# Kernel tuning notes

Hardware: AMD Instinct MI355X
Metric: run time of the kernel (lower is better)

The kernel has to match this reference:

```python
import jax, jax.numpy as jnp
import numpy as np

N_OUT, D_OUT, N_IN, D_IN, N_ROUTING = 32, 32, 2048, 16, 3
BATCH = 64


def squash(x, axis=-1):
    norm2 = jnp.sum(x * x, axis=axis, keepdims=True)
    scale = norm2 / (1.0 + norm2) / jnp.sqrt(norm2)
    return scale * x


def setup_inputs() -> dict:
    key = jax.random.key(0)
    k_u, k_w = jax.random.split(key)
    u = jax.random.normal(k_u, (BATCH, N_IN, D_IN), dtype=jnp.float32)
    stdv = 1.0 / np.sqrt(N_IN)
    W = jax.random.uniform(k_w, (N_IN, D_IN, N_OUT * D_OUT), dtype=jnp.float32,
                           minval=-stdv, maxval=stdv)
    return {"u": u, "W": W}


def reference(u, W):
    B = u.shape[0]
    # uhat[b,n,o,k] = sum_i u[b,n,i] * W[n,i,o*k]
    uhat = jnp.einsum('bni,nij->bnj', u, W).reshape(B, N_IN, N_OUT, D_OUT)
    b = jnp.zeros((B, N_IN, N_OUT), dtype=u.dtype)
    v = None
    for r in range(N_ROUTING):
        c = jax.nn.softmax(b, axis=-1)            # [B, nIn, nOut]
        s = jnp.einsum('bno,bnok->bok', c, uhat)  # [B, nOut, dOut]
        v = squash(s)
        if r != N_ROUTING - 1:
            a = jnp.einsum('bnok,bok->bno', uhat, v)  # agreement
            b = b + a
    return v
```

## Files before the change

### kernel.cpp

```cpp
#include <hip/hip_runtime.h>
#include <math.h>

#define N_OUT 32
#define D_OUT 32
#define N_IN 2048
#define D_IN 16
#define BATCH 64
#define J 1024

typedef __attribute__((ext_vector_type(8))) short short8;
typedef __attribute__((ext_vector_type(4))) float f32x4;
typedef __attribute__((ext_vector_type(16))) float f32x16;

__device__ __forceinline__ unsigned short f2bf(float f) {
  unsigned int x = __float_as_uint(f);
  return (unsigned short)((x + 0x7FFFu + ((x >> 16) & 1u)) >> 16);
}

__device__ __forceinline__ int wp(int u) { return u ^ ((u >> 3) & 1); }

__device__ __forceinline__ void pack_col(const float* wc, uint4& d0, uint4& d1) {
  d0.x = (unsigned)f2bf(wc[0])  | ((unsigned)f2bf(wc[1])  << 16);
  d0.y = (unsigned)f2bf(wc[2])  | ((unsigned)f2bf(wc[3])  << 16);
  d0.z = (unsigned)f2bf(wc[4])  | ((unsigned)f2bf(wc[5])  << 16);
  d0.w = (unsigned)f2bf(wc[6])  | ((unsigned)f2bf(wc[7])  << 16);
  d1.x = (unsigned)f2bf(wc[8])  | ((unsigned)f2bf(wc[9])  << 16);
  d1.y = (unsigned)f2bf(wc[10]) | ((unsigned)f2bf(wc[11]) << 16);
  d1.z = (unsigned)f2bf(wc[12]) | ((unsigned)f2bf(wc[13]) << 16);
  d1.w = (unsigned)f2bf(wc[14]) | ((unsigned)f2bf(wc[15]) << 16);
}

__device__ __forceinline__ short8 pack_u(const float4& a4, const float4& b4) {
  short8 B;
  B[0] = (short)f2bf(a4.x); B[1] = (short)f2bf(a4.y);
  B[2] = (short)f2bf(a4.z); B[3] = (short)f2bf(a4.w);
  B[4] = (short)f2bf(b4.x); B[5] = (short)f2bf(b4.y);
  B[6] = (short)f2bf(b4.z); B[7] = (short)f2bf(b4.w);
  return B;
}

__device__ __forceinline__ f32x16 zero16() {
  f32x16 z;
  #pragma unroll
  for (int i = 0; i < 16; ++i) z[i] = 0.f;
  return z;
}


template<int MODE>
__global__ __launch_bounds__(1024, 1)
void pass0w_kernel(const float* __restrict__ uf, const float* __restrict__ Wf,
                   short* __restrict__ Wbf, short* __restrict__ ubf,
                   float* __restrict__ part)
{
  __shared__ uint4 Wt[4][2048];

  const int t  = threadIdx.x;
  const int l  = t & 63;
  const int w  = t >> 6;
  const int bid = blockIdx.x;
  const int bh = (bid >> 3) & 1;
  const int cx = (bid & 7) | ((bid >> 4) << 3);
  const int n0 = cx * 16;

  const int bl = l & 31;
  const int b  = bh * 32 + bl;
  const int kh = l >> 5;
  const bool wq = (MODE == 0) && ((t >> 9) == bh);
  const bool uq = (MODE == 0) && (w == 0);

  int aoff[2];
  #pragma unroll
  for (int q = 0; q < 2; ++q) aoff[q] = wp(2 * (w * 64 + q * 32 + bl) + kh);

  f32x16 acc[2];
  acc[0] = zero16();
  acc[1] = zero16();

  short8 Ba, Bb;

  {
    float wa[16], wb[16];
    const float* sa = Wf + (size_t)n0 * (D_IN * J) + t;
    const float* sb = Wf + (size_t)(n0 + 1) * (D_IN * J) + t;
    #pragma unroll
    for (int i = 0; i < 16; ++i) wa[i] = sa[i * J];
    #pragma unroll
    for (int i = 0; i < 16; ++i) wb[i] = sb[i * J];
    const float* upa = uf + ((size_t)b * N_IN + n0) * D_IN + kh * 8;
    float4 ua0 = *reinterpret_cast<const float4*>(upa);
    float4 ua1 = *reinterpret_cast<const float4*>(upa + 4);
    const float* upb = uf + ((size_t)b * N_IN + n0 + 1) * D_IN + kh * 8;
    float4 ub0 = *reinterpret_cast<const float4*>(upb);
    float4 ub1 = *reinterpret_cast<const float4*>(upb + 4);
    __builtin_amdgcn_sched_barrier(0);
    uint4 d0, d1;
    pack_col(wa, d0, d1);
    Wt[0][wp(2 * t)] = d0;
    Wt[0][wp(2 * t + 1)] = d1;
    if (wq) {
      uint4* g = reinterpret_cast<uint4*>(Wbf + (size_t)n0 * (D_IN * J));
      g[wp(2 * t)] = d0;
      g[wp(2 * t + 1)] = d1;
    }
    pack_col(wb, d0, d1);
    Wt[1][wp(2 * t)] = d0;
    Wt[1][wp(2 * t + 1)] = d1;
    if (wq) {
      uint4* g = reinterpret_cast<uint4*>(Wbf + (size_t)(n0 + 1) * (D_IN * J));
      g[wp(2 * t)] = d0;
      g[wp(2 * t + 1)] = d1;
    }
    Ba = pack_u(ua0, ua1);
    Bb = pack_u(ub0, ub1);
    if (uq) {
      *reinterpret_cast<short8*>(ubf + ((size_t)b * N_IN + n0) * D_IN + kh * 8) = Ba;
      *reinterpret_cast<short8*>(ubf + ((size_t)b * N_IN + n0 + 1) * D_IN + kh * 8) = Bb;
    }
  }
  __syncthreads();

  for (int ss = 0; ss < 8; ++ss) {
    const int na = n0 + 2 * ss;
    const int p = ss & 1;
    const bool more = (ss + 1 < 8);

    float wa[16], wb[16];
    float4 ua0 = {0,0,0,0}, ua1 = {0,0,0,0}, ub0 = {0,0,0,0}, ub1 = {0,0,0,0};
    if (more) {
      const float* sa = Wf + (size_t)(na + 2) * (D_IN * J) + t;
      const float* sb = Wf + (size_t)(na + 3) * (D_IN * J) + t;
      #pragma unroll
      for (int i = 0; i < 16; ++i) wa[i] = sa[i * J];
      #pragma unroll
      for (int i = 0; i < 16; ++i) wb[i] = sb[i * J];
      const float* upa = uf + ((size_t)b * N_IN + na + 2) * D_IN + kh * 8;
      ua0 = *reinterpret_cast<const float4*>(upa);
      ua1 = *reinterpret_cast<const float4*>(upa + 4);
      const float* upb = uf + ((size_t)b * N_IN + na + 3) * D_IN + kh * 8;
      ub0 = *reinterpret_cast<const float4*>(upb);
      ub1 = *reinterpret_cast<const float4*>(upb + 4);
      __builtin_amdgcn_sched_barrier(0);
    }

    {
      const uint4* bufA = Wt[2 * p];
      const uint4* bufB = Wt[2 * p + 1];
      #pragma unroll
      for (int q = 0; q < 2; ++q) {
        short8 A = *reinterpret_cast<const short8*>(&bufA[aoff[q]]);
        acc[q] = __builtin_amdgcn_mfma_f32_32x32x16_bf16(A, Ba, acc[q], 0, 0, 0);
      }
      #pragma unroll
      for (int q = 0; q < 2; ++q) {
        short8 A = *reinterpret_cast<const short8*>(&bufB[aoff[q]]);
        acc[q] = __builtin_amdgcn_mfma_f32_32x32x16_bf16(A, Bb, acc[q], 0, 0, 0);
      }
    }

    short8 Bna, Bnb;
    if (more) {
      uint4 d0, d1;
      pack_col(wa, d0, d1);
      Wt[2 * (1 - p)][wp(2 * t)] = d0;
      Wt[2 * (1 - p)][wp(2 * t + 1)] = d1;
      if (wq) {
        uint4* g = reinterpret_cast<uint4*>(Wbf + (size_t)(na + 2) * (D_IN * J));
        g[wp(2 * t)] = d0;
        g[wp(2 * t + 1)] = d1;
      }
      pack_col(wb, d0, d1);
      Wt[2 * (1 - p) + 1][wp(2 * t)] = d0;
      Wt[2 * (1 - p) + 1][wp(2 * t + 1)] = d1;
      if (wq) {
        uint4* g = reinterpret_cast<uint4*>(Wbf + (size_t)(na + 3) * (D_IN * J));
        g[wp(2 * t)] = d0;
        g[wp(2 * t + 1)] = d1;
      }
      Bna = pack_u(ua0, ua1);
      Bnb = pack_u(ub0, ub1);
      if (uq) {
        *reinterpret_cast<short8*>(ubf + ((size_t)b * N_IN + na + 2) * D_IN + kh * 8) = Bna;
        *reinterpret_cast<short8*>(ubf + ((size_t)b * N_IN + na + 3) * D_IN + kh * 8) = Bnb;
      }
      Ba = Bna;
      Bb = Bnb;
    }
    __syncthreads();
  }

  #pragma unroll
  for (int q = 0; q < 2; ++q) {
    #pragma unroll
    for (int r = 0; r < 16; ++r) {
      int j = w * 64 + q * 32 + (r & 3) + 8 * (r >> 2) + 4 * kh;
      part[((size_t)cx * J + j) * 64 + b] = acc[q][r];
    }
  }
}

__global__ __launch_bounds__(1024, 1)
void pass1w_kernel(const short* __restrict__ Wbf, const short* __restrict__ ubf,
                   const float* __restrict__ vin, float* __restrict__ part)
{
  __shared__ uint4 Wt[2][2048];
  __shared__ float al[2][32][33];

  const int t  = threadIdx.x;
  const int l  = t & 63;
  const int w  = t >> 6;
  const int bid = blockIdx.x;
  const int bh = (bid >> 3) & 1;
  const int cx = (bid & 7) | ((bid >> 4) << 3);
  const int n0 = cx * 16;

  const int bl = l & 31;
  const int b  = bh * 32 + bl;
  const int kh = l >> 5;

  int aoff[2];
  #pragma unroll
  for (int q = 0; q < 2; ++q) aoff[q] = wp(2 * (w * 64 + q * 32 + bl) + kh);

  unsigned vb[16];
  #pragma unroll
  for (int q = 0; q < 2; ++q) {
    #pragma unroll
    for (int g = 0; g < 4; ++g) {
      int j = w * 64 + q * 32 + 8 * g + 4 * kh;
      f32x4 v4 = *reinterpret_cast<const f32x4*>(vin + (size_t)b * J + j);
      vb[q * 8 + 2 * g]     = (unsigned)f2bf(v4[0]) | ((unsigned)f2bf(v4[1]) << 16);
      vb[q * 8 + 2 * g + 1] = (unsigned)f2bf(v4[2]) | ((unsigned)f2bf(v4[3]) << 16);
    }
  }

  f32x16 acc[2];
  acc[0] = zero16();
  acc[1] = zero16();

  short8 B;
  {
    const uint4* src = reinterpret_cast<const uint4*>(Wbf + (size_t)n0 * (D_IN * J));
    Wt[0][t] = src[t];
    Wt[0][t + 1024] = src[t + 1024];
    B = *reinterpret_cast<const short8*>(ubf + ((size_t)b * N_IN + n0) * D_IN + kh * 8);
  }
  __syncthreads();

  for (int nn = 0; nn < 16; ++nn) {
    const int n = n0 + nn;
    const int cur = nn & 1, nxt = cur ^ 1, par = nn & 1;
    const bool more = (nn + 1 < 16);

    uint4 s0, s1;
    short8 Bn;
    if (more) {
      const uint4* src = reinterpret_cast<const uint4*>(Wbf + (size_t)(n + 1) * (D_IN * J));
      s0 = src[t];
      s1 = src[t + 1024];
      Bn = *reinterpret_cast<const short8*>(ubf + ((size_t)b * N_IN + n + 1) * D_IN + kh * 8);
      __builtin_amdgcn_sched_barrier(0);
    }

    f32x16 C[2];
    {
      const uint4* buf = Wt[cur];
      #pragma unroll
      for (int q = 0; q < 2; ++q) {
        short8 A = *reinterpret_cast<const short8*>(&buf[aoff[q]]);
        C[q] = __builtin_amdgcn_mfma_f32_32x32x16_bf16(A, B, zero16(), 0, 0, 0);
      }
    }

    #pragma unroll
    for (int q = 0; q < 2; ++q) {
      float s = 0.f;
      #pragma unroll
      for (int r = 0; r < 16; ++r) {
        unsigned u = vb[q * 8 + (r >> 1)];
        float v = (r & 1) ? __uint_as_float(u & 0xffff0000u)
                          : __uint_as_float(u << 16);
        s += C[q][r] * v;
      }
      s += __shfl_xor(s, 32);
      if (l < 32) al[par][w * 2 + q][bl] = s;
    }

    if (more) {
      Wt[nxt][t] = s0;
      Wt[nxt][t + 1024] = s1;
    }

    __syncthreads();
    {
      int sb = t >> 5, so = t & 31;
      float x = al[par][so][sb];
      float m = x;
      #pragma unroll
      for (int k = 1; k < 32; k <<= 1) m = fmaxf(m, __shfl_xor(m, k));
      float e = __expf(x - m);
      float sm = e;
      #pragma unroll
      for (int k = 1; k < 32; k <<= 1) sm += __shfl_xor(sm, k);
      al[par][so][sb] = e / sm;
    }
    __syncthreads();
    #pragma unroll
    for (int q = 0; q < 2; ++q) {
      float c = al[par][w * 2 + q][bl];
      #pragma unroll
      for (int r = 0; r < 16; ++r) acc[q][r] += C[q][r] * c;
    }
    B = Bn;
  }

  #pragma unroll
  for (int q = 0; q < 2; ++q) {
    #pragma unroll
    for (int r = 0; r < 16; ++r) {
      int j = w * 64 + q * 32 + (r & 3) + 8 * (r >> 2) + 4 * kh;
      part[((size_t)cx * J + j) * 64 + b] = acc[q][r];
    }
  }
}

template<bool HAS_V, int MODE, int NCHUNK>
__global__ __launch_bounds__(1024, 1)
void pass_kernel(const float* __restrict__ uf, const float* __restrict__ Wf,
                 short* __restrict__ Wbf, short* __restrict__ ubf,
                 const float* __restrict__ vin, float* __restrict__ part)
{
  __shared__ uint4 Wt[2][2048];
  __shared__ float al[2][32][18];

  const int t  = threadIdx.x;
  const int l  = t & 63;
  const int w  = t >> 6;
  const int bid = blockIdx.x;
  const int bq = (bid >> 3) & 3;
  const int cx = (bid & 7) | ((bid >> 5) << 3);
  const int n0 = cx * NCHUNK;

  const int bl = l & 15;
  const int b  = bq * 16 + bl;
  const int h  = l >> 4;
  const int hA = h & 1;
  const bool ld = (l < 32);

  f32x4 vf[4];
  if (HAS_V) {
    #pragma unroll
    for (int q = 0; q < 4; ++q)
      vf[q] = *reinterpret_cast<const f32x4*>(vin + (size_t)b * J + (w*4+q)*16 + h*4);
  }

  int aoff[4];
  #pragma unroll
  for (int q = 0; q < 4; ++q) aoff[q] = wp(2 * ((w*4+q) * 16 + bl) + hA);

  f32x4 acc[4];
  #pragma unroll
  for (int q = 0; q < 4; ++q) acc[q] = f32x4{0.f, 0.f, 0.f, 0.f};

  short8 Bcur = short8{0,0,0,0,0,0,0,0};
  {
    float wc[16];
    const float* wsrc = Wf + (size_t)n0 * (D_IN * J) + t;
    #pragma unroll
    for (int i = 0; i < 16; ++i) wc[i] = wsrc[i * J];
    float4 a4 = {0,0,0,0}, b4 = {0,0,0,0};
    if (ld) {
      const float* up = uf + ((size_t)b * N_IN + n0) * D_IN + hA * 8;
      a4 = *reinterpret_cast<const float4*>(up);
      b4 = *reinterpret_cast<const float4*>(up + 4);
    }
    __builtin_amdgcn_sched_barrier(0);
    uint4 d0, d1;
    pack_col(wc, d0, d1);
    Wt[0][wp(2 * t)] = d0;
    Wt[0][wp(2 * t + 1)] = d1;
    if (ld) Bcur = pack_u(a4, b4);
  }
  __syncthreads();

  for (int nn = 0; nn < NCHUNK; ++nn) {
    const int n = n0 + nn;
    const int cur = nn & 1, nxt = cur ^ 1, par = nn & 1;
    const bool more = (nn + 1 < NCHUNK);

    float wc[16];
    float4 a4 = {0,0,0,0}, b4 = {0,0,0,0};
    if (more) {
      const float* wsrc = Wf + (size_t)(n + 1) * (D_IN * J) + t;
      #pragma unroll
      for (int i = 0; i < 16; ++i) wc[i] = wsrc[i * J];
      if (ld) {
        const float* up = uf + ((size_t)b * N_IN + n + 1) * D_IN + hA * 8;
        a4 = *reinterpret_cast<const float4*>(up);
        b4 = *reinterpret_cast<const float4*>(up + 4);
      }
      __builtin_amdgcn_sched_barrier(0);
    }

    f32x4 C[4];
    const uint4* buf = Wt[cur];
    #pragma unroll
    for (int q = 0; q < 4; ++q) {
      short8 A = short8{0,0,0,0,0,0,0,0};
      if (ld) A = *reinterpret_cast<const short8*>(&buf[aoff[q]]);
      f32x4 z = f32x4{0.f, 0.f, 0.f, 0.f};
      C[q] = __builtin_amdgcn_mfma_f32_16x16x32_bf16(A, Bcur, z, 0, 0, 0);
    }

    short8 Bn = short8{0,0,0,0,0,0,0,0};
    if (more && ld) Bn = pack_u(a4, b4);

    if (HAS_V) {
      float ap[2] = {0.f, 0.f};
      #pragma unroll
      for (int q = 0; q < 4; ++q) {
        float s = C[q][0]*vf[q][0] + C[q][1]*vf[q][1] + C[q][2]*vf[q][2] + C[q][3]*vf[q][3];
        ap[q >> 1] += s;
      }
      #pragma unroll
      for (int p = 0; p < 2; ++p) {
        float s = ap[p];
        s += __shfl_xor(s, 16);
        s += __shfl_xor(s, 32);
        if (l < 16) al[par][w * 2 + p][l] = s;
      }
      if (more) {
        uint4 d0, d1;
        pack_col(wc, d0, d1);
        Wt[nxt][wp(2 * t)] = d0;
        Wt[nxt][wp(2 * t + 1)] = d1;
      }
      __syncthreads();
      if (t < 512) {
        int sb = t >> 5, so = t & 31;
        float x = al[par][so][sb];
        float m = x;
        #pragma unroll
        for (int k = 1; k < 32; k <<= 1) m = fmaxf(m, __shfl_xor(m, k));
        float e = __expf(x - m);
        float sm = e;
        #pragma unroll
        for (int k = 1; k < 32; k <<= 1) sm += __shfl_xor(sm, k);
        al[par][so][sb] = e / sm;
      }
      __syncthreads();
      #pragma unroll
      for (int q = 0; q < 4; ++q) {
        float c = al[par][(w * 4 + q) >> 1][bl];
        acc[q] += C[q] * c;
      }
    } else {
      #pragma unroll
      for (int q = 0; q < 4; ++q) acc[q] += C[q];
      if (more) {
        uint4 d0, d1;
        pack_col(wc, d0, d1);
        Wt[nxt][wp(2 * t)] = d0;
        Wt[nxt][wp(2 * t + 1)] = d1;
      }
      __syncthreads();
    }
    Bcur = Bn;
  }

  #pragma unroll
  for (int q = 0; q < 4; ++q) {
    int jbase = (w * 4 + q) * 16 + h * 4;
    #pragma unroll
    for (int r = 0; r < 4; ++r)
      part[((size_t)cx * J + jbase + r) * 64 + b] = acc[q][r];
  }
}

template<int NC>
__global__ __launch_bounds__(1024)
void rsq_kernel(const float* __restrict__ part, const float* __restrict__ addv,
                float* __restrict__ out, float prescale)
{
  __shared__ float ps[2][32][17];
  __shared__ float vl[32][17];
  __shared__ float scl[16];
  const int o  = blockIdx.x >> 2;
  const int bq = blockIdx.x & 3;
  const int t  = threadIdx.x;
  {
    const int bb = t & 15;
    const int kk = (t >> 4) & 31;
    const int ch = t >> 9;
    const float* p = part + (size_t)(o * 32 + kk) * 64 + bq * 16 + bb;
    float s = 0.f;
    #pragma unroll 8
    for (int c = ch * (NC / 2); c < (ch + 1) * (NC / 2); ++c)
      s += p[(size_t)c * (J * 64)];
    ps[ch][kk][bb] = s;
  }
  __syncthreads();
  if (t < 512) {
    int kk = t >> 4, bb = t & 15;
    vl[kk][bb] = (ps[0][kk][bb] + ps[1][kk][bb]) * prescale;
  }
  __syncthreads();
  if (t < 16) {
    float n2 = 0.f;
    #pragma unroll
    for (int k = 0; k < 32; ++k) { float x = vl[k][t]; n2 += x * x; }
    scl[t] = sqrtf(n2) / (1.f + n2);
  }
  __syncthreads();
  if (t < 512) {
    int bb = t >> 5, kk = t & 31;
    int idx = (bq * 16 + bb) * J + o * 32 + kk;
    float val = scl[bb] * vl[kk][bb];
    if (addv) val += addv[idx];
    out[idx] = val;
  }
}

extern "C" void kernel_launch(void* const* d_in, const int* in_sizes, int n_in,
                              void* d_out, int out_size, void* d_ws, size_t ws_size,
                              hipStream_t stream)
{
  const float* u = (const float*)d_in[0];
  const float* W = (const float*)d_in[1];
  float* out = (float*)d_out;
  char* ws = (char*)d_ws;

  const size_t WBF_B = (size_t)N_IN * D_IN * J * 2;
  const size_t UBF_B = (size_t)BATCH * N_IN * D_IN * 2;
  const size_t SMALL = 2ull * BATCH * J * 4;
  const size_t PART128 = (size_t)128 * J * 64 * 4;
  const size_t PART64  = (size_t)64 * J * 64 * 4;

  if (ws_size >= WBF_B + UBF_B + PART128 + SMALL) {
    short* Wbf = (short*)ws;
    short* ubf = (short*)(ws + WBF_B);
    float* part = (float*)(ws + WBF_B + UBF_B);
    float* v0 = part + (size_t)128 * J * 64;
    float* vs = v0 + BATCH * J;
    pass0w_kernel<0><<<256, 1024, 0, stream>>>(u, W, Wbf, ubf, part);
    rsq_kernel<128><<<128, 1024, 0, stream>>>(part, nullptr, v0, 1.f / 32.f);
    pass1w_kernel<<<256, 1024, 0, stream>>>(Wbf, ubf, v0, part);
    rsq_kernel<128><<<128, 1024, 0, stream>>>(part, v0, vs, 1.f);
    pass1w_kernel<<<256, 1024, 0, stream>>>(Wbf, ubf, vs, part);
    rsq_kernel<128><<<128, 1024, 0, stream>>>(part, nullptr, out, 1.f);
  } else if (ws_size >= PART64 + SMALL) {
    float* part = (float*)ws;
    float* v0 = part + (size_t)64 * J * 64;
    float* vs = v0 + BATCH * J;
    pass_kernel<false, 2, 32><<<256, 1024, 0, stream>>>(u, W, nullptr, nullptr, nullptr, part);
    rsq_kernel<64><<<128, 1024, 0, stream>>>(part, nullptr, v0, 1.f / 32.f);
    pass_kernel<true, 2, 32><<<256, 1024, 0, stream>>>(u, W, nullptr, nullptr, v0, part);
    rsq_kernel<64><<<128, 1024, 0, stream>>>(part, v0, vs, 1.f);
    pass_kernel<true, 2, 32><<<256, 1024, 0, stream>>>(u, W, nullptr, nullptr, vs, part);
    rsq_kernel<64><<<128, 1024, 0, stream>>>(part, nullptr, out, 1.f);
  } else {
    float* part = (float*)ws;
    float* v0 = part + (size_t)16 * J * 64;
    float* vs = v0 + BATCH * J;
    pass_kernel<false, 2, 128><<<64, 1024, 0, stream>>>(u, W, nullptr, nullptr, nullptr, part);
    rsq_kernel<16><<<128, 1024, 0, stream>>>(part, nullptr, v0, 1.f / 32.f);
    pass_kernel<true, 2, 128><<<64, 1024, 0, stream>>>(u, W, nullptr, nullptr, v0, part);
    rsq_kernel<16><<<128, 1024, 0, stream>>>(part, v0, vs, 1.f);
    pass_kernel<true, 2, 128><<<64, 1024, 0, stream>>>(u, W, nullptr, nullptr, vs, part);
    rsq_kernel<16><<<128, 1024, 0, stream>>>(part, nullptr, out, 1.f);
  }
}
```

Measured before the change: 159.3 us.

## Replace LDS-staged pass0 with small-block wave-shuffle kernel over 1024 blocks

```diff
diff --git a/kernel.cpp b/kernel.cpp
--- a/kernel.cpp
+++ b/kernel.cpp
@@ -46,154 +46,92 @@
   return z;
 }
 
-
-template<int MODE>
-__global__ __launch_bounds__(1024, 1)
-void pass0w_kernel(const float* __restrict__ uf, const float* __restrict__ Wf,
+template<int NCHUNK>
+__global__ __launch_bounds__(256, 4)
+void pass0s_kernel(const float* __restrict__ uf, const float* __restrict__ Wf,
                    short* __restrict__ Wbf, short* __restrict__ ubf,
                    float* __restrict__ part)
 {
-  __shared__ uint4 Wt[4][2048];
-
-  const int t  = threadIdx.x;
-  const int l  = t & 63;
-  const int w  = t >> 6;
+  const int t   = threadIdx.x;
+  const int l   = t & 63;
+  const int wv  = t >> 6;
   const int bid = blockIdx.x;
-  const int bh = (bid >> 3) & 1;
-  const int cx = (bid & 7) | ((bid >> 4) << 3);
-  const int n0 = cx * 16;
-
-  const int bl = l & 31;
-  const int b  = bh * 32 + bl;
-  const int kh = l >> 5;
-  const bool wq = (MODE == 0) && ((t >> 9) == bh);
-  const bool uq = (MODE == 0) && (w == 0);
-
-  int aoff[2];
-  #pragma unroll
-  for (int q = 0; q < 2; ++q) aoff[q] = wp(2 * (w * 64 + q * 32 + bl) + kh);
+  const int bjg = bid & 3;
+  const int bh  = (bid >> 2) & 1;
+  const int cx  = bid >> 3;
+  const int jg  = bjg * 4 + wv;
+  const int j0  = jg * 64;
+  const int bl  = l & 31;
+  const int b   = bh * 32 + bl;
+  const int kh  = l >> 5;
+  const int n0  = cx * NCHUNK;
+  const bool emitW = (bh == 0);
+  const bool emitU = (jg == 0);
 
   f32x16 acc[2];
   acc[0] = zero16();
   acc[1] = zero16();
 
-  short8 Ba, Bb;
-
-  {
-    float wa[16], wb[16];
-    const float* sa = Wf + (size_t)n0 * (D_IN * J) + t;
-    const float* sb = Wf + (size_t)(n0 + 1) * (D_IN * J) + t;
-    #pragma unroll
-    for (int i = 0; i < 16; ++i) wa[i] = sa[i * J];
-    #pragma unroll
-    for (int i = 0; i < 16; ++i) wb[i] = sb[i * J];
-    const float* upa = uf + ((size_t)b * N_IN + n0) * D_IN + kh * 8;
-    float4 ua0 = *reinterpret_cast<const float4*>(upa);
-    float4 ua1 = *reinterpret_cast<const float4*>(upa + 4);
-    const float* upb = uf + ((size_t)b * N_IN + n0 + 1) * D_IN + kh * 8;
-    float4 ub0 = *reinterpret_cast<const float4*>(upb);
-    float4 ub1 = *reinterpret_cast<const float4*>(upb + 4);
-    __builtin_amdgcn_sched_barrier(0);
+  float wcA[16], wcB[16];
+  float4 uA0, uA1, uB0, uB1;
+
+  auto load_n = [&](float (&wc)[16], float4& u0, float4& u1, int n) {
+    const float* ws = Wf + (size_t)n * (D_IN * J) + j0 + l;
+    #pragma unroll
+    for (int i = 0; i < 16; ++i) wc[i] = ws[i * J];
+    const float* up = uf + ((size_t)b * N_IN + n) * D_IN + kh * 8;
+    u0 = *reinterpret_cast<const float4*>(up);
+    u1 = *reinterpret_cast<const float4*>(up + 4);
+  };
+
+  auto body = [&](const float (&wc)[16], const float4& u0, const float4& u1, int n) {
     uint4 d0, d1;
-    pack_col(wa, d0, d1);
-    Wt[0][wp(2 * t)] = d0;
-    Wt[0][wp(2 * t + 1)] = d1;
-    if (wq) {
-      uint4* g = reinterpret_cast<uint4*>(Wbf + (size_t)n0 * (D_IN * J));
-      g[wp(2 * t)] = d0;
-      g[wp(2 * t + 1)] = d1;
-    }
-    pack_col(wb, d0, d1);
-    Wt[1][wp(2 * t)] = d0;
-    Wt[1][wp(2 * t + 1)] = d1;
-    if (wq) {
-      uint4* g = reinterpret_cast<uint4*>(Wbf + (size_t)(n0 + 1) * (D_IN * J));
-      g[wp(2 * t)] = d0;
-      g[wp(2 * t + 1)] = d1;
-    }
-    Ba = pack_u(ua0, ua1);
-    Bb = pack_u(ub0, ub1);
-    if (uq) {
-      *reinterpret_cast<short8*>(ubf + ((size_t)b * N_IN + n0) * D_IN + kh * 8) = Ba;
-      *reinterpret_cast<short8*>(ubf + ((size_t)b * N_IN + n0 + 1) * D_IN + kh * 8) = Bb;
-    }
-  }
-  __syncthreads();
-
-  for (int ss = 0; ss < 8; ++ss) {
-    const int na = n0 + 2 * ss;
-    const int p = ss & 1;
-    const bool more = (ss + 1 < 8);
-
-    float wa[16], wb[16];
-    float4 ua0 = {0,0,0,0}, ua1 = {0,0,0,0}, ub0 = {0,0,0,0}, ub1 = {0,0,0,0};
-    if (more) {
-      const float* sa = Wf + (size_t)(na + 2) * (D_IN * J) + t;
-      const float* sb = Wf + (size_t)(na + 3) * (D_IN * J) + t;
-      #pragma unroll
-      for (int i = 0; i < 16; ++i) wa[i] = sa[i * J];
-      #pragma unroll
-      for (int i = 0; i < 16; ++i) wb[i] = sb[i * J];
-      const float* upa = uf + ((size_t)b * N_IN + na + 2) * D_IN + kh * 8;
-      ua0 = *reinterpret_cast<const float4*>(upa);
-      ua1 = *reinterpret_cast<const float4*>(upa + 4);
-      const float* upb = uf + ((size_t)b * N_IN + na + 3) * D_IN + kh * 8;
-      ub0 = *reinterpret_cast<const float4*>(upb);
-      ub1 = *reinterpret_cast<const float4*>(upb + 4);
+    pack_col(wc, d0, d1);
+    if (emitW) {
+      uint4* g = reinterpret_cast<uint4*>(Wbf + (size_t)n * (D_IN * J));
+      g[wp(2 * (j0 + l))] = d0;
+      g[wp(2 * (j0 + l) + 1)] = d1;
+    }
+    short8 B = pack_u(u0, u1);
+    if (emitU)
+      *reinterpret_cast<short8*>(ubf + ((size_t)b * N_IN + n) * D_IN + kh * 8) = B;
+    const unsigned* p0 = reinterpret_cast<const unsigned*>(&d0);
+    const unsigned* p1 = reinterpret_cast<const unsigned*>(&d1);
+    #pragma unroll
+    for (int q = 0; q < 2; ++q) {
+      int src = q * 32 + bl;
+      unsigned a[4];
+      #pragma unroll
+      for (int e = 0; e < 4; ++e) {
+        unsigned lo = (unsigned)__shfl((int)p0[e], src);
+        unsigned hi = (unsigned)__shfl((int)p1[e], src);
+        a[e] = kh ? hi : lo;
+      }
+      short8 A = *reinterpret_cast<const short8*>(a);
+      acc[q] = __builtin_amdgcn_mfma_f32_32x32x16_bf16(A, B, acc[q], 0, 0, 0);
+    }
+  };
+
+  load_n(wcA, uA0, uA1, n0);
+
+  #pragma unroll
+  for (int ss = 0; ss < NCHUNK; ++ss) {
+    const int n = n0 + ss;
+    const bool cur_is_A = ((ss & 1) == 0);
+    if (ss + 1 < NCHUNK) {
+      if (cur_is_A) load_n(wcB, uB0, uB1, n + 1);
+      else          load_n(wcA, uA0, uA1, n + 1);
       __builtin_amdgcn_sched_barrier(0);
     }
-
-    {
-      const uint4* bufA = Wt[2 * p];
-      const uint4* bufB = Wt[2 * p + 1];
-      #pragma unroll
-      for (int q = 0; q < 2; ++q) {
-        short8 A = *reinterpret_cast<const short8*>(&bufA[aoff[q]]);
-        acc[q] = __builtin_amdgcn_mfma_f32_32x32x16_bf16(A, Ba, acc[q], 0, 0, 0);
-      }
-      #pragma unroll
-      for (int q = 0; q < 2; ++q) {
-        short8 A = *reinterpret_cast<const short8*>(&bufB[aoff[q]]);
-        acc[q] = __builtin_amdgcn_mfma_f32_32x32x16_bf16(A, Bb, acc[q], 0, 0, 0);
-      }
-    }
-
-    short8 Bna, Bnb;
-    if (more) {
-      uint4 d0, d1;
-      pack_col(wa, d0, d1);
-      Wt[2 * (1 - p)][wp(2 * t)] = d0;
-      Wt[2 * (1 - p)][wp(2 * t + 1)] = d1;
-      if (wq) {
-        uint4* g = reinterpret_cast<uint4*>(Wbf + (size_t)(na + 2) * (D_IN * J));
-        g[wp(2 * t)] = d0;
-        g[wp(2 * t + 1)] = d1;
-      }
-      pack_col(wb, d0, d1);
-      Wt[2 * (1 - p) + 1][wp(2 * t)] = d0;
-      Wt[2 * (1 - p) + 1][wp(2 * t + 1)] = d1;
-      if (wq) {
-        uint4* g = reinterpret_cast<uint4*>(Wbf + (size_t)(na + 3) * (D_IN * J));
-        g[wp(2 * t)] = d0;
-        g[wp(2 * t + 1)] = d1;
-      }
-      Bna = pack_u(ua0, ua1);
-      Bnb = pack_u(ub0, ub1);
-      if (uq) {
-        *reinterpret_cast<short8*>(ubf + ((size_t)b * N_IN + na + 2) * D_IN + kh * 8) = Bna;
-        *reinterpret_cast<short8*>(ubf + ((size_t)b * N_IN + na + 3) * D_IN + kh * 8) = Bnb;
-      }
-      Ba = Bna;
-      Bb = Bnb;
-    }
-    __syncthreads();
+    if (cur_is_A) body(wcA, uA0, uA1, n);
+    else          body(wcB, uB0, uB1, n);
   }
 
   #pragma unroll
   for (int q = 0; q < 2; ++q) {
     #pragma unroll
     for (int r = 0; r < 16; ++r) {
-      int j = w * 64 + q * 32 + (r & 3) + 8 * (r >> 2) + 4 * kh;
+      int j = j0 + q * 32 + (r & 3) + 8 * (r >> 2) + 4 * kh;
       part[((size_t)cx * J + j) * 64 + b] = acc[q][r];
     }
   }
@@ -542,7 +480,7 @@
     float* part = (float*)(ws + WBF_B + UBF_B);
     float* v0 = part + (size_t)128 * J * 64;
     float* vs = v0 + BATCH * J;
-    pass0w_kernel<0><<<256, 1024, 0, stream>>>(u, W, Wbf, ubf, part);
+    pass0s_kernel<16><<<1024, 256, 0, stream>>>(u, W, Wbf, ubf, part);
     rsq_kernel<128><<<128, 1024, 0, stream>>>(part, nullptr, v0, 1.f / 32.f);
     pass1w_kernel<<<256, 1024, 0, stream>>>(Wbf, ubf, v0, part);
     rsq_kernel<128><<<128, 1024, 0, stream>>>(part, v0, vs, 1.f);
```

New measurement: 197.5 us. 1.24x slower.

## Fuse routing passes into one cooperative persistent kernel with grid syncs

Applied to the files above, without the earlier changes.

```diff
diff --git a/kernel.cpp b/kernel.cpp
--- a/kernel.cpp
+++ b/kernel.cpp
@@ -1,5 +1,8 @@
 #include <hip/hip_runtime.h>
+#include <hip/hip_cooperative_groups.h>
 #include <math.h>
+
+namespace cg = cooperative_groups;
 
 #define N_OUT 32
 #define D_OUT 32
@@ -47,14 +50,12 @@
 }
 
 
-template<int MODE>
-__global__ __launch_bounds__(1024, 1)
-void pass0w_kernel(const float* __restrict__ uf, const float* __restrict__ Wf,
-                   short* __restrict__ Wbf, short* __restrict__ ubf,
-                   float* __restrict__ part)
-{
-  __shared__ uint4 Wt[4][2048];
-
+
+__device__ __forceinline__
+void pass0_phase(const float* __restrict__ uf, const float* __restrict__ Wf,
+                 short* __restrict__ Wbf, short* __restrict__ ubf,
+                 float* __restrict__ part, uint4 (&Wt)[4][2048])
+{
   const int t  = threadIdx.x;
   const int l  = t & 63;
   const int w  = t >> 6;
@@ -66,8 +67,8 @@
   const int bl = l & 31;
   const int b  = bh * 32 + bl;
   const int kh = l >> 5;
-  const bool wq = (MODE == 0) && ((t >> 9) == bh);
-  const bool uq = (MODE == 0) && (w == 0);
+  const bool wq = ((t >> 9) == bh);
+  const bool uq = (w == 0);
 
   int aoff[2];
   #pragma unroll
@@ -199,13 +200,11 @@
   }
 }
 
-__global__ __launch_bounds__(1024, 1)
-void pass1w_kernel(const short* __restrict__ Wbf, const short* __restrict__ ubf,
-                   const float* __restrict__ vin, float* __restrict__ part)
-{
-  __shared__ uint4 Wt[2][2048];
-  __shared__ float al[2][32][33];
-
+__device__ __forceinline__
+void pass1_phase(const short* __restrict__ Wbf, const short* __restrict__ ubf,
+                 const float* __restrict__ vin, float* __restrict__ part,
+                 uint4 (&Wt)[4][2048], float (&al)[2][32][33])
+{
   const int t  = threadIdx.x;
   const int l  = t & 63;
   const int w  = t >> 6;
@@ -324,169 +323,15 @@
   }
 }
 
-template<bool HAS_V, int MODE, int NCHUNK>
-__global__ __launch_bounds__(1024, 1)
-void pass_kernel(const float* __restrict__ uf, const float* __restrict__ Wf,
-                 short* __restrict__ Wbf, short* __restrict__ ubf,
-                 const float* __restrict__ vin, float* __restrict__ part)
-{
-  __shared__ uint4 Wt[2][2048];
-  __shared__ float al[2][32][18];
-
-  const int t  = threadIdx.x;
-  const int l  = t & 63;
-  const int w  = t >> 6;
+__device__ __forceinline__
+void rsq_phase(const float* __restrict__ part, const float* __restrict__ addv,
+               float* __restrict__ out, float prescale,
+               float (&ps)[2][32][17], float (&vl)[32][17], float (&scl)[16])
+{
   const int bid = blockIdx.x;
-  const int bq = (bid >> 3) & 3;
-  const int cx = (bid & 7) | ((bid >> 5) << 3);
-  const int n0 = cx * NCHUNK;
-
-  const int bl = l & 15;
-  const int b  = bq * 16 + bl;
-  const int h  = l >> 4;
-  const int hA = h & 1;
-  const bool ld = (l < 32);
-
-  f32x4 vf[4];
-  if (HAS_V) {
-    #pragma unroll
-    for (int q = 0; q < 4; ++q)
-      vf[q] = *reinterpret_cast<const f32x4*>(vin + (size_t)b * J + (w*4+q)*16 + h*4);
-  }
-
-  int aoff[4];
-  #pragma unroll
-  for (int q = 0; q < 4; ++q) aoff[q] = wp(2 * ((w*4+q) * 16 + bl) + hA);
-
-  f32x4 acc[4];
-  #pragma unroll
-  for (int q = 0; q < 4; ++q) acc[q] = f32x4{0.f, 0.f, 0.f, 0.f};
-
-  short8 Bcur = short8{0,0,0,0,0,0,0,0};
-  {
-    float wc[16];
-    const float* wsrc = Wf + (size_t)n0 * (D_IN * J) + t;
-    #pragma unroll
-    for (int i = 0; i < 16; ++i) wc[i] = wsrc[i * J];
-    float4 a4 = {0,0,0,0}, b4 = {0,0,0,0};
-    if (ld) {
-      const float* up = uf + ((size_t)b * N_IN + n0) * D_IN + hA * 8;
-      a4 = *reinterpret_cast<const float4*>(up);
-      b4 = *reinterpret_cast<const float4*>(up + 4);
-    }
-    __builtin_amdgcn_sched_barrier(0);
-    uint4 d0, d1;
-    pack_col(wc, d0, d1);
-    Wt[0][wp(2 * t)] = d0;
-    Wt[0][wp(2 * t + 1)] = d1;
-    if (ld) Bcur = pack_u(a4, b4);
-  }
-  __syncthreads();
-
-  for (int nn = 0; nn < NCHUNK; ++nn) {
-    const int n = n0 + nn;
-    const int cur = nn & 1, nxt = cur ^ 1, par = nn & 1;
-    const bool more = (nn + 1 < NCHUNK);
-
-    float wc[16];
-    float4 a4 = {0,0,0,0}, b4 = {0,0,0,0};
-    if (more) {
-      const float* wsrc = Wf + (size_t)(n + 1) * (D_IN * J) + t;
-      #pragma unroll
-      for (int i = 0; i < 16; ++i) wc[i] = wsrc[i * J];
-      if (ld) {
-        const float* up = uf + ((size_t)b * N_IN + n + 1) * D_IN + hA * 8;
-        a4 = *reinterpret_cast<const float4*>(up);
-        b4 = *reinterpret_cast<const float4*>(up + 4);
-      }
-      __builtin_amdgcn_sched_barrier(0);
-    }
-
-    f32x4 C[4];
-    const uint4* buf = Wt[cur];
-    #pragma unroll
-    for (int q = 0; q < 4; ++q) {
-      short8 A = short8{0,0,0,0,0,0,0,0};
-      if (ld) A = *reinterpret_cast<const short8*>(&buf[aoff[q]]);
-      f32x4 z = f32x4{0.f, 0.f, 0.f, 0.f};
-      C[q] = __builtin_amdgcn_mfma_f32_16x16x32_bf16(A, Bcur, z, 0, 0, 0);
-    }
-
-    short8 Bn = short8{0,0,0,0,0,0,0,0};
-    if (more && ld) Bn = pack_u(a4, b4);
-
-    if (HAS_V) {
-      float ap[2] = {0.f, 0.f};
-      #pragma unroll
-      for (int q = 0; q < 4; ++q) {
-        float s = C[q][0]*vf[q][0] + C[q][1]*vf[q][1] + C[q][2]*vf[q][2] + C[q][3]*vf[q][3];
-        ap[q >> 1] += s;
-      }
-      #pragma unroll
-      for (int p = 0; p < 2; ++p) {
-        float s = ap[p];
-        s += __shfl_xor(s, 16);
-        s += __shfl_xor(s, 32);
-        if (l < 16) al[par][w * 2 + p][l] = s;
-      }
-      if (more) {
-        uint4 d0, d1;
-        pack_col(wc, d0, d1);
-        Wt[nxt][wp(2 * t)] = d0;
-        Wt[nxt][wp(2 * t + 1)] = d1;
-      }
-      __syncthreads();
-      if (t < 512) {
-        int sb = t >> 5, so = t & 31;
-        float x = al[par][so][sb];
-        float m = x;
-        #pragma unroll
-        for (int k = 1; k < 32; k <<= 1) m = fmaxf(m, __shfl_xor(m, k));
-        float e = __expf(x - m);
-        float sm = e;
-        #pragma unroll
-        for (int k = 1; k < 32; k <<= 1) sm += __shfl_xor(sm, k);
-        al[par][so][sb] = e / sm;
-      }
-      __syncthreads();
-      #pragma unroll
-      for (int q = 0; q < 4; ++q) {
-        float c = al[par][(w * 4 + q) >> 1][bl];
-        acc[q] += C[q] * c;
-      }
-    } else {
-      #pragma unroll
-      for (int q = 0; q < 4; ++q) acc[q] += C[q];
-      if (more) {
-        uint4 d0, d1;
-        pack_col(wc, d0, d1);
-        Wt[nxt][wp(2 * t)] = d0;
-        Wt[nxt][wp(2 * t + 1)] = d1;
-      }
-      __syncthreads();
-    }
-    Bcur = Bn;
-  }
-
-  #pragma unroll
-  for (int q = 0; q < 4; ++q) {
-    int jbase = (w * 4 + q) * 16 + h * 4;
-    #pragma unroll
-    for (int r = 0; r < 4; ++r)
-      part[((size_t)cx * J + jbase + r) * 64 + b] = acc[q][r];
-  }
-}
-
-template<int NC>
-__global__ __launch_bounds__(1024)
-void rsq_kernel(const float* __restrict__ part, const float* __restrict__ addv,
-                float* __restrict__ out, float prescale)
-{
-  __shared__ float ps[2][32][17];
-  __shared__ float vl[32][17];
-  __shared__ float scl[16];
-  const int o  = blockIdx.x >> 2;
-  const int bq = blockIdx.x & 3;
+  if (bid >= 128) return;
+  const int o  = bid >> 2;
+  const int bq = bid & 3;
   const int t  = threadIdx.x;
   {
     const int bb = t & 15;
@@ -495,7 +340,7 @@
     const float* p = part + (size_t)(o * 32 + kk) * 64 + bq * 16 + bb;
     float s = 0.f;
     #pragma unroll 8
-    for (int c = ch * (NC / 2); c < (ch + 1) * (NC / 2); ++c)
+    for (int c = ch * 64; c < (ch + 1) * 64; ++c)
       s += p[(size_t)c * (J * 64)];
     ps[ch][kk][bb] = s;
   }
@@ -519,6 +364,62 @@
     if (addv) val += addv[idx];
     out[idx] = val;
   }
+  __syncthreads();
+}
+
+__global__ __launch_bounds__(1024)
+void mega_kernel(const float* __restrict__ uf, const float* __restrict__ Wf,
+                 short* __restrict__ Wbf, short* __restrict__ ubf,
+                 float* __restrict__ part, float* __restrict__ v0,
+                 float* __restrict__ vs, float* __restrict__ out)
+{
+  __shared__ uint4 Wt[4][2048];
+  __shared__ float al[2][32][33];
+  __shared__ float ps[2][32][17];
+  __shared__ float vl[32][17];
+  __shared__ float scl[16];
+
+  cg::grid_group grid = cg::this_grid();
+
+  pass0_phase(uf, Wf, Wbf, ubf, part, Wt);
+  grid.sync();
+  rsq_phase(part, nullptr, v0, 1.f / 32.f, ps, vl, scl);
+  grid.sync();
+  pass1_phase(Wbf, ubf, v0, part, Wt, al);
+  grid.sync();
+  rsq_phase(part, v0, vs, 1.f, ps, vl, scl);
+  grid.sync();
+  pass1_phase(Wbf, ubf, vs, part, Wt, al);
+  grid.sync();
+  rsq_phase(part, nullptr, out, 1.f, ps, vl, scl);
+}
+
+__global__ __launch_bounds__(1024, 1)
+void pass0w_kernel(const float* __restrict__ uf, const float* __restrict__ Wf,
+                   short* __restrict__ Wbf, short* __restrict__ ubf,
+                   float* __restrict__ part)
+{
+  __shared__ uint4 Wt[4][2048];
+  pass0_phase(uf, Wf, Wbf, ubf, part, Wt);
+}
+
+__global__ __launch_bounds__(1024, 1)
+void pass1w_kernel(const short* __restrict__ Wbf, const short* __restrict__ ubf,
+                   const float* __restrict__ vin, float* __restrict__ part)
+{
+  __shared__ uint4 Wt[4][2048];
+  __shared__ float al[2][32][33];
+  pass1_phase(Wbf, ubf, vin, part, Wt, al);
+}
+
+__global__ __launch_bounds__(1024)
+void rsq_kernel(const float* __restrict__ part, const float* __restrict__ addv,
+                float* __restrict__ out, float prescale)
+{
+  __shared__ float ps[2][32][17];
+  __shared__ float vl[32][17];
+  __shared__ float scl[16];
+  rsq_phase(part, addv, out, prescale, ps, vl, scl);
 }
 
 extern "C" void kernel_launch(void* const* d_in, const int* in_sizes, int n_in,
@@ -534,7 +435,6 @@
   const size_t UBF_B = (size_t)BATCH * N_IN * D_IN * 2;
   const size_t SMALL = 2ull * BATCH * J * 4;
   const size_t PART128 = (size_t)128 * J * 64 * 4;
-  const size_t PART64  = (size_t)64 * J * 64 * 4;
 
   if (ws_size >= WBF_B + UBF_B + PART128 + SMALL) {
     short* Wbf = (short*)ws;
@@ -542,31 +442,32 @@
     float* part = (float*)(ws + WBF_B + UBF_B);
     float* v0 = part + (size_t)128 * J * 64;
     float* vs = v0 + BATCH * J;
-    pass0w_kernel<0><<<256, 1024, 0, stream>>>(u, W, Wbf, ubf, part);
-    rsq_kernel<128><<<128, 1024, 0, stream>>>(part, nullptr, v0, 1.f / 32.f);
+
+    void* args[] = {(void*)&u, (void*)&W, (void*)&Wbf, (void*)&ubf,
+                    (void*)&part, (void*)&v0, (void*)&vs, (void*)&out};
+    hipError_t err = hipLaunchCooperativeKernel((const void*)mega_kernel,
+                                                dim3(256), dim3(1024),
+                                                args, 0, stream);
+    if (err != hipSuccess) {
+      (void)hipGetLastError();
+      pass0w_kernel<<<256, 1024, 0, stream>>>(u, W, Wbf, ubf, part);
+      rsq_kernel<<<128, 1024, 0, stream>>>(part, nullptr, v0, 1.f / 32.f);
+      pass1w_kernel<<<256, 1024, 0, stream>>>(Wbf, ubf, v0, part);
+      rsq_kernel<<<128, 1024, 0, stream>>>(part, v0, vs, 1.f);
+      pass1w_kernel<<<256, 1024, 0, stream>>>(Wbf, ubf, vs, part);
+      rsq_kernel<<<128, 1024, 0, stream>>>(part, nullptr, out, 1.f);
+    }
+  } else {
+    short* Wbf = (short*)ws;
+    short* ubf = (short*)(ws + WBF_B);
+    float* part = (float*)(ws + WBF_B + UBF_B);
+    float* v0 = part + (size_t)128 * J * 64;
+    float* vs = v0 + BATCH * J;
+    pass0w_kernel<<<256, 1024, 0, stream>>>(u, W, Wbf, ubf, part);
+    rsq_kernel<<<128, 1024, 0, stream>>>(part, nullptr, v0, 1.f / 32.f);
     pass1w_kernel<<<256, 1024, 0, stream>>>(Wbf, ubf, v0, part);
-    rsq_kernel<128><<<128, 1024, 0, stream>>>(part, v0, vs, 1.f);
+    rsq_kernel<<<128, 1024, 0, stream>>>(part, v0, vs, 1.f);
     pass1w_kernel<<<256, 1024, 0, stream>>>(Wbf, ubf, vs, part);
-    rsq_kernel<128><<<128, 1024, 0, stream>>>(part, nullptr, out, 1.f);
-  } else if (ws_size >= PART64 + SMALL) {
-    float* part = (float*)ws;
-    float* v0 = part + (size_t)64 * J * 64;
-    float* vs = v0 + BATCH * J;
-    pass_kernel<false, 2, 32><<<256, 1024, 0, stream>>>(u, W, nullptr, nullptr, nullptr, part);
-    rsq_kernel<64><<<128, 1024, 0, stream>>>(part, nullptr, v0, 1.f / 32.f);
-    pass_kernel<true, 2, 32><<<256, 1024, 0, stream>>>(u, W, nullptr, nullptr, v0, part);
-    rsq_kernel<64><<<128, 1024, 0, stream>>>(part, v0, vs, 1.f);
-    pass_kernel<true, 2, 32><<<256, 1024, 0, stream>>>(u, W, nullptr, nullptr, vs, part);
-    rsq_kernel<64><<<128, 1024, 0, stream>>>(part, nullptr, out, 1.f);
-  } else {
-    float* part = (float*)ws;
-    float* v0 = part + (size_t)16 * J * 64;
-    float* vs = v0 + BATCH * J;
-    pass_kernel<false, 2, 128><<<64, 1024, 0, stream>>>(u, W, nullptr, nullptr, nullptr, part);
-    rsq_kernel<16><<<128, 1024, 0, stream>>>(part, nullptr, v0, 1.f / 32.f);
-    pass_kernel<true, 2, 128><<<64, 1024, 0, stream>>>(u, W, nullptr, nullptr, v0, part);
-    rsq_kernel<16><<<128, 1024, 0, stream>>>(part, v0, vs, 1.f);
-    pass_kernel<true, 2, 128><<<64, 1024, 0, stream>>>(u, W, nullptr, nullptr, vs, part);
-    rsq_kernel<16><<<128, 1024, 0, stream>>>(part, nullptr, out, 1.f);
-  }
-}
+    rsq_kernel<<<128, 1024, 0, stream>>>(part, nullptr, out, 1.f);
+  }
+}
```

Result: slower. 402.5 us (+152.7%).
